# Optimization experiments

Hardware: AMD Instinct MI355X
Metric: run time of the kernel (lower is better)

## Reference

```python
import jax, jax.numpy as jnp
import numpy as np
from jax import lax

EPS = 1e-07
B, H, W = 32, 120, 120
N_PRIM, PRIM_DIM = 16, 8          # 16 capsule types, 8-d pose
N_SEC, SEC_DIM = 10, 16           # 10 secondary capsules, 16-d
FLAT = 9216                       # 16 * 24 * 24
R_ITERS = 3
REC_DIM = H * W * 3               # 43200


def _conv(x, w, b, stride):
    # NHWC input, HWIO kernel, VALID padding
    y = lax.conv_general_dilated(x, w, (stride, stride), 'VALID',
                                 dimension_numbers=('NHWC', 'HWIO', 'NHWC'))
    return y + b


def _squash(s):
    s_norm = jnp.linalg.norm(s, axis=-1, keepdims=True)
    sq = jnp.square(s_norm)
    return sq / (1.0 + sq) * s / (s_norm + EPS)


def setup_inputs() -> dict:
    key = jax.random.key(0)
    ks = jax.random.split(key, 13)
    p = lambda k, shp, s=0.05: (jax.random.normal(k, shp, dtype=jnp.float32) * s)
    inp = {
        'input_x': jax.random.normal(ks[0], (B, H, W, 3), dtype=jnp.float32),
        'y':       jax.random.uniform(ks[1], (B, N_SEC), dtype=jnp.float32),
        'conv1_w': p(ks[2], (9, 9, 3, 256)),
        'conv1_b': jnp.zeros((256,), jnp.float32),
        'conv2_w': p(ks[3], (9, 9, 256, N_PRIM * PRIM_DIM)),
        'conv2_b': jnp.zeros((N_PRIM * PRIM_DIM,), jnp.float32),
        'w_pose':  p(ks[4], (1, FLAT, N_SEC, SEC_DIM, PRIM_DIM)),
        'w1': p(ks[5], (N_SEC * SEC_DIM, 512)), 'b1': jnp.zeros((512,), jnp.float32),
        'w2': p(ks[6], (512, 1024)),            'b2': jnp.zeros((1024,), jnp.float32),
        'w3': p(ks[7], (1024, REC_DIM)),        'b3': jnp.zeros((REC_DIM,), jnp.float32),
    }
    return inp


def reference(input_x, y, conv1_w, conv1_b, conv2_w, conv2_b, w_pose,
              w1, b1, w2, b2, w3, b3):
    b = input_x.shape[0]
    # feature extraction
    x = jax.nn.relu(_conv(input_x, conv1_w, conv1_b, 2))   # [B,56,56,256]
    x = _conv(x, conv2_w, conv2_b, 2)                      # [B,24,24,128]
    u = x.reshape(b, FLAT, PRIM_DIM)                       # [B,9216,8]
    # u_hat[b,n,c,d] = sum_p w_pose[0,n,c,d,p] * u[b,n,p]
    u_hat = jnp.einsum('ncdp,bnp->bncd', w_pose[0], u)     # [B,9216,10,16]
    # dynamic routing
    logits = jnp.zeros((b, FLAT, N_SEC, 1), jnp.float32)
    v = None
    for _ in range(R_ITERS):
        c = jax.nn.softmax(logits, axis=-2)                # over secondary caps
        s = jnp.sum(c * u_hat, axis=1, keepdims=True)      # [B,1,10,16]
        v = _squash(s)
        agreement = jnp.sum(u_hat * v, axis=-1, keepdims=True)  # [B,9216,10,1]
        logits = logits + agreement
    # masking + reconstruction
    mask = y[:, None, :, None]                             # [B,1,10,1]
    v_flat = (mask * v).reshape(b, -1)                     # [B,160]
    h = jax.nn.relu(v_flat @ w1 + b1)
    h = jax.nn.relu(h @ w2 + b2)
    rec = jax.nn.sigmoid(h @ w3 + b3)                      # [B,43200]
    return v, rec
```

## Files before the change

kernel.cpp:

```cpp
#include <hip/hip_runtime.h>
#include <hip/hip_bf16.h>

typedef unsigned short u16;
typedef unsigned int   u32;
typedef __attribute__((ext_vector_type(8))) __bf16 bf16x8;
typedef __attribute__((ext_vector_type(4))) float  f32x4;

#define EPSQ 1e-7f
#define KSPLIT 9
#define KPB 2304
#define KSTEPS 72
#define FC3SPL 8

#define GLDS16(gp, lp) __builtin_amdgcn_global_load_lds( \
    (const __attribute__((address_space(1))) void*)(gp), \
    (__attribute__((address_space(3))) void*)(lp), 16, 0, 0)

__device__ __forceinline__ u16 f2bf(float f){
  u32 u = __float_as_uint(f);
  u32 r = (u + 0x7fffu + ((u >> 16) & 1u)) >> 16;
  return (u16)r;
}
__device__ __forceinline__ float bf2f(u16 h){ return __uint_as_float(((u32)h) << 16); }
__device__ __forceinline__ float blo(u32 w){ return __uint_as_float(w << 16); }
__device__ __forceinline__ float bhi(u32 w){ return __uint_as_float(w & 0xffff0000u); }

__global__ __launch_bounds__(256) void k_im2col(const float* __restrict__ x, u16* __restrict__ A1){
  const int id = blockIdx.x*256 + threadIdx.x;
  const int m  = id >> 5;
  const int s  = id & 31;
  const int b  = m / 3136;
  const int r  = m - b*3136;
  const int oy = r / 56;
  const int ox = r - oy*56;
  const float* xb = x + ((size_t)b*120 + 2*oy)*120*3 + 2*ox*3;
  u16 vals[8];
  #pragma unroll
  for (int j=0;j<8;++j){
    int k = s*8 + j;
    if (k < 243){
      int ky = k / 27;
      int rem = k - ky*27;
      vals[j] = f2bf(xb[(size_t)ky*360 + rem]);
    } else vals[j] = 0;
  }
  *reinterpret_cast<uint4*>(A1 + (size_t)m*256 + s*8) = *reinterpret_cast<uint4*>(vals);
}

__global__ __launch_bounds__(256) void k_wt1(const float* __restrict__ w, u16* __restrict__ wt){
  __shared__ float tile[32][33];
  const int k0 = blockIdx.x*32;
  const int c0 = blockIdx.y*32;
  const int c  = threadIdx.x & 31;
  const int r8 = threadIdx.x >> 5;
  #pragma unroll
  for (int rr=0; rr<4; ++rr){
    int r = r8*4+rr;
    tile[r][c] = (k0+r < 243) ? w[(size_t)(k0+r)*256 + c0 + c] : 0.f;
  }
  __syncthreads();
  #pragma unroll
  for (int rr=0; rr<4; ++rr){
    int r = r8*4+rr;
    wt[(size_t)(c0+r)*256 + k0 + c] = f2bf(tile[c][r]);
  }
}

__global__ __launch_bounds__(256) void k_gemm1(const u16* __restrict__ A1,
    const u16* __restrict__ w1t, const float* __restrict__ bias, u16* __restrict__ a1b){
  __shared__ __align__(16) u16 As[2][4096];
  __shared__ __align__(16) u16 Bs[2][4096];
  const int t  = threadIdx.x;
  const int bx = blockIdx.x;
  const int by = blockIdx.y;
  const int row0 = t>>2, slot = t&3;
  const int wid = t>>6, lane = t&63;
  const int wr = wid>>1, wc = wid&1, lr = lane&15, lq = lane>>4;
  const size_t srcA0 = (size_t)(bx*128 + row0)*256 + slot*8;
  const size_t srcA1 = srcA0 + (size_t)64*256;
  const size_t srcB0 = (size_t)(by*128 + row0)*256 + slot*8;
  const size_t srcB1 = srcB0 + (size_t)64*256;
  f32x4 acc[4][4];
  #pragma unroll
  for (int i=0;i<4;++i)
    #pragma unroll
    for (int j=0;j<4;++j) acc[i][j] = (f32x4){0.f,0.f,0.f,0.f};

  auto stage = [&](int step, int buf){
    const int k0 = step*32;
    GLDS16(A1 + srcA0 + k0, &As[buf][wid*512]);
    GLDS16(A1 + srcA1 + k0, &As[buf][wid*512 + 2048]);
    GLDS16(w1t + srcB0 + k0, &Bs[buf][wid*512]);
    GLDS16(w1t + srcB1 + k0, &Bs[buf][wid*512 + 2048]);
  };
  auto compute = [&](int buf){
    bf16x8 af[4], bfv[4];
    #pragma unroll
    for (int mi=0;mi<4;++mi)
      af[mi] = *reinterpret_cast<const bf16x8*>(&As[buf][(wr*64 + mi*16 + lr)*32 + lq*8]);
    #pragma unroll
    for (int ni=0;ni<4;++ni)
      bfv[ni] = *reinterpret_cast<const bf16x8*>(&Bs[buf][(wc*64 + ni*16 + lr)*32 + lq*8]);
    #pragma unroll
    for (int mi=0;mi<4;++mi)
      #pragma unroll
      for (int ni=0;ni<4;++ni)
        acc[mi][ni] = __builtin_amdgcn_mfma_f32_16x16x32_bf16(af[mi], bfv[ni], acc[mi][ni], 0, 0, 0);
  };

  stage(0, 0);
  int cur = 0;
  for (int step=0; step<8; ++step){
    if (step+1 < 8){
      stage(step+1, cur^1);
      asm volatile("s_waitcnt vmcnt(4)" ::: "memory");
    } else {
      asm volatile("s_waitcnt vmcnt(0)" ::: "memory");
    }
    __builtin_amdgcn_s_barrier();
    __builtin_amdgcn_sched_barrier(0);
    compute(cur);
    __builtin_amdgcn_s_barrier();
    __builtin_amdgcn_sched_barrier(0);
    cur ^= 1;
  }

  #pragma unroll
  for (int ni=0;ni<4;++ni){
    int colg = by*128 + wc*64 + ni*16 + lr;
    float bv = bias[colg];
    #pragma unroll
    for (int mi=0;mi<4;++mi){
      #pragma unroll
      for (int r=0;r<4;++r){
        int rowg = bx*128 + wr*64 + mi*16 + lq*4 + r;
        float v = fmaxf(acc[mi][ni][r] + bv, 0.f);
        a1b[(size_t)rowg*256 + colg] = f2bf(v);
      }
    }
  }
}

__global__ __launch_bounds__(256) void k_wt(const float* __restrict__ w, u16* __restrict__ wt){
  __shared__ float tile[32][33];
  const int k0 = blockIdx.x*32;
  const int c0 = blockIdx.y*32;
  const int c  = threadIdx.x & 31;
  const int r8 = threadIdx.x >> 5;
  #pragma unroll
  for (int rr=0; rr<4; ++rr){
    int r = r8*4+rr;
    tile[r][c] = w[(size_t)(k0+r)*128 + c0 + c];
  }
  __syncthreads();
  #pragma unroll
  for (int rr=0; rr<4; ++rr){
    int r = r8*4+rr;
    wt[(size_t)(c0+r)*20736 + k0 + c] = f2bf(tile[c][r]);
  }
}

__global__ __launch_bounds__(256) void k_conv2(const u16* __restrict__ a1b,
    const u16* __restrict__ w2t, float* __restrict__ part){
  __shared__ __align__(16) u16 As[2][4096];
  __shared__ __align__(16) u16 Bs[2][4096];
  const int t  = threadIdx.x;
  const int bx = blockIdx.x;
  const int ks = blockIdx.y;
  const int row0 = t>>2, slot = t&3;
  int gA[2]; int gB[2];
  #pragma unroll
  for (int q=0;q<2;++q){
    int m  = bx*128 + row0 + q*64;
    int bb = m/576; int r = m - bb*576; int oy = r/24; int ox = r - oy*24;
    gA[q] = ((bb*56 + 2*oy)*56 + 2*ox)*256 + slot*8;
    int col = row0 + q*64;
    gB[q] = col*20736 + slot*8;
  }
  const int wid = t>>6, lane = t&63;
  const int wr = wid>>1, wc = wid&1, lr = lane&15, lq = lane>>4;
  f32x4 acc[4][4];
  #pragma unroll
  for (int i=0;i<4;++i)
    #pragma unroll
    for (int j=0;j<4;++j) acc[i][j] = (f32x4){0.f,0.f,0.f,0.f};
  const int kbase = ks*KPB;

  auto stage = [&](int step, int buf){
    const int k0  = kbase + step*32;
    const int kk  = k0 >> 8;
    const int ky  = kk/9;
    const int kx  = kk - ky*9;
    const int ic0 = k0 & 255;
    const int soff = (ky*56 + kx)*256 + ic0;
    GLDS16(a1b + gA[0] + soff, &As[buf][wid*512]);
    GLDS16(a1b + gA[1] + soff, &As[buf][wid*512 + 2048]);
    GLDS16(w2t + gB[0] + k0,  &Bs[buf][wid*512]);
    GLDS16(w2t + gB[1] + k0,  &Bs[buf][wid*512 + 2048]);
  };
  auto compute = [&](int buf){
    bf16x8 af[4], bfv[4];
    #pragma unroll
    for (int mi=0;mi<4;++mi)
      af[mi] = *reinterpret_cast<const bf16x8*>(&As[buf][(wr*64 + mi*16 + lr)*32 + lq*8]);
    #pragma unroll
    for (int ni=0;ni<4;++ni)
      bfv[ni] = *reinterpret_cast<const bf16x8*>(&Bs[buf][(wc*64 + ni*16 + lr)*32 + lq*8]);
    #pragma unroll
    for (int mi=0;mi<4;++mi)
      #pragma unroll
      for (int ni=0;ni<4;++ni)
        acc[mi][ni] = __builtin_amdgcn_mfma_f32_16x16x32_bf16(af[mi], bfv[ni], acc[mi][ni], 0, 0, 0);
  };

  stage(0, 0);
  int cur = 0;
  for (int step=0; step<KSTEPS; ++step){
    if (step+1 < KSTEPS){
      stage(step+1, cur^1);
      asm volatile("s_waitcnt vmcnt(4)" ::: "memory");
    } else {
      asm volatile("s_waitcnt vmcnt(0)" ::: "memory");
    }
    __builtin_amdgcn_s_barrier();
    __builtin_amdgcn_sched_barrier(0);
    compute(cur);
    __builtin_amdgcn_s_barrier();
    __builtin_amdgcn_sched_barrier(0);
    cur ^= 1;
  }

  const size_t base = ((size_t)ks*18432 + (size_t)bx*128)*128;
  #pragma unroll
  for (int mi=0;mi<4;++mi){
    #pragma unroll
    for (int ni=0;ni<4;++ni){
      int col = wc*64 + ni*16 + lr;
      #pragma unroll
      for (int r=0;r<4;++r){
        int row = wr*64 + mi*16 + lq*4 + r;
        part[base + (size_t)row*128 + col] = acc[mi][ni][r];
      }
    }
  }
}

__global__ __launch_bounds__(256) void k_comb(const float* __restrict__ part,
    const float* __restrict__ bias, float* __restrict__ u){
  const int i4 = blockIdx.x*256 + threadIdx.x;
  const float4* b4 = reinterpret_cast<const float4*>(bias);
  float4 s = b4[i4 & 31];
  const float4* p4 = reinterpret_cast<const float4*>(part);
  #pragma unroll
  for (int ks=0; ks<KSPLIT; ++ks){
    float4 p = p4[(size_t)ks*589824 + i4];
    s.x += p.x; s.y += p.y; s.z += p.z; s.w += p.w;
  }
  reinterpret_cast<float4*>(u)[i4] = s;
}

__global__ __launch_bounds__(256) void k_uhat(const float* __restrict__ u,
    const float* __restrict__ wpose, u16* __restrict__ uhat){
  __shared__ float Wn[1280];
  __shared__ float us[256];
  const int n = blockIdx.x;
  const int t = threadIdx.x;
  #pragma unroll
  for (int j=0;j<5;++j) Wn[t + j*256] = wpose[(size_t)n*1280 + t + j*256];
  us[t] = u[((size_t)(t>>3)*9216 + n)*8 + (t&7)];
  __syncthreads();
  const int b = t>>3, d0 = (t&7)*2;
  float uv[8];
  #pragma unroll
  for (int p=0;p<8;++p) uv[p] = us[b*8+p];
  for (int c=0;c<10;++c){
    const float* w0 = &Wn[(c*16 + d0)*8];
    float v0=0.f, v1=0.f;
    #pragma unroll
    for (int p=0;p<8;++p){ v0 = fmaf(w0[p], uv[p], v0); v1 = fmaf(w0[8+p], uv[p], v1); }
    u32 pk = (u32)f2bf(v0) | ((u32)f2bf(v1) << 16);
    *reinterpret_cast<u32*>(uhat + ((((size_t)b*10 + c)*9216 + n)*16 + d0)) = pk;
  }
}

template<int ITER>
__global__ __launch_bounds__(256) void k_route(const u16* __restrict__ uhat,
    const float* __restrict__ spin, float* __restrict__ logi,
    float* __restrict__ spout){
  const int ch = blockIdx.x;
  const int b  = blockIdx.y;
  const int t  = threadIdx.x;
  const int n  = ch*256 + t;
  __shared__ float vl[160];
  __shared__ float sq[160];
  __shared__ float wlds[10][257];
  __shared__ float pacc[10][16][33];
  if (ITER >= 2){
    float sv = 0.f;
    if (t < 160){
      #pragma unroll 4
      for (int c2=0;c2<36;++c2) sv += spin[((size_t)c2*32 + b)*160 + t];
      sq[t] = sv*sv;
    }
    __syncthreads();
    if (t < 160){
      int cc = t >> 4;
      float ss = 0.f;
      #pragma unroll
      for (int j=0;j<16;++j) ss += sq[cc*16 + j];
      float nrm = sqrtf(ss);
      vl[t] = (ss/(1.f+ss)) * sv / (nrm + EPSQ);
    }
    __syncthreads();
  }
  float w[10];
  if (ITER == 1){
    #pragma unroll
    for (int c=0;c<10;++c) w[c] = 0.1f;
  } else {
    float l[10];
    #pragma unroll
    for (int c=0;c<10;++c){
      const u16* up = uhat + ((((size_t)b*10 + c)*9216 + n) << 4);
      const uint4 q0 = *reinterpret_cast<const uint4*>(up);
      const uint4 q1 = *reinterpret_cast<const uint4*>(up + 8);
      const float* v = &vl[c*16];
      float dot = blo(q0.x)*v[0] + bhi(q0.x)*v[1]
                + blo(q0.y)*v[2] + bhi(q0.y)*v[3]
                + blo(q0.z)*v[4] + bhi(q0.z)*v[5]
                + blo(q0.w)*v[6] + bhi(q0.w)*v[7]
                + blo(q1.x)*v[8] + bhi(q1.x)*v[9]
                + blo(q1.y)*v[10]+ bhi(q1.y)*v[11]
                + blo(q1.z)*v[12]+ bhi(q1.z)*v[13]
                + blo(q1.w)*v[14]+ bhi(q1.w)*v[15];
      size_t li = ((size_t)b*10 + c)*9216 + n;
      float lc = dot;
      if (ITER == 3) lc += logi[li];
      if (ITER == 2) logi[li] = lc;
      l[c] = lc;
    }
    float mx = l[0];
    #pragma unroll
    for (int c=1;c<10;++c) mx = fmaxf(mx, l[c]);
    float s = 0.f;
    #pragma unroll
    for (int c=0;c<10;++c){ w[c] = __expf(l[c]-mx); s += w[c]; }
    float inv = 1.f/s;
    #pragma unroll
    for (int c=0;c<10;++c) w[c] *= inv;
  }
  #pragma unroll
  for (int c=0;c<10;++c) wlds[c][t] = w[c];
  __syncthreads();

  const int nl = t>>3, dp = t&7;
  float a0[10], a1[10];
  #pragma unroll
  for (int c=0;c<10;++c){ a0[c]=0.f; a1[c]=0.f; }
  #pragma unroll
  for (int c=0;c<10;++c){
    const u32* ub = reinterpret_cast<const u32*>(
        uhat + ((((size_t)b*10 + c)*9216 + (size_t)ch*256) << 4));
    float acc0 = 0.f, acc1 = 0.f;
    #pragma unroll
    for (int chunk=0; chunk<8; ++chunk){
      u32 v = ub[chunk*256 + t];
      float wv = wlds[c][chunk*32 + nl];
      acc0 = fmaf(wv, blo(v), acc0);
      acc1 = fmaf(wv, bhi(v), acc1);
    }
    a0[c] = acc0; a1[c] = acc1;
  }
  #pragma unroll
  for (int c=0;c<10;++c){
    pacc[c][2*dp  ][nl] = a0[c];
    pacc[c][2*dp+1][nl] = a1[c];
  }
  __syncthreads();
  if (t < 160){
    const int c = t >> 4, d = t & 15;
    float acc = 0.f;
    #pragma unroll
    for (int j=0;j<32;++j) acc += pacc[c][d][j];
    spout[((size_t)ch*32 + b)*160 + t] = acc;
  }
}

__global__ __launch_bounds__(256) void k_head(const float* __restrict__ y,
    const float* __restrict__ spin, const float* __restrict__ w1,
    const float* __restrict__ b1, const float* __restrict__ w2,
    const float* __restrict__ b2, float* __restrict__ dout_v,
    float* __restrict__ h2T){
  const int b = blockIdx.x;
  const int q = blockIdx.y;
  const int t = threadIdx.x;
  __shared__ float vl[160];
  __shared__ float sq[160];
  __shared__ float h1s[512];
  float sv = 0.f;
  if (t < 160){
    #pragma unroll 4
    for (int c2=0;c2<36;++c2) sv += spin[((size_t)c2*32 + b)*160 + t];
    sq[t] = sv*sv;
  }
  __syncthreads();
  if (t < 160){
    int cc = t >> 4;
    float ss = 0.f;
    #pragma unroll
    for (int j=0;j<16;++j) ss += sq[cc*16 + j];
    float nrm = sqrtf(ss);
    float vv = (ss/(1.f+ss)) * sv / (nrm + EPSQ);
    if (q == 0) dout_v[(size_t)b*160 + t] = vv;
    vl[t] = vv * y[b*10 + cc];
  }
  __syncthreads();
  #pragma unroll
  for (int j=0;j<2;++j){
    const int oc = j*256 + t;
    float acc = b1[oc];
    for (int k=0;k<160;++k) acc = fmaf(vl[k], w1[(size_t)k*512 + oc], acc);
    h1s[oc] = fmaxf(acc, 0.f);
  }
  __syncthreads();
  const int oc2 = q*256 + t;
  float acc = b2[oc2];
  for (int k=0;k<512;++k) acc = fmaf(h1s[k], w2[(size_t)k*1024 + oc2], acc);
  h2T[(size_t)oc2*32 + b] = fmaxf(acc, 0.f);
}

__global__ __launch_bounds__(256) void k_fc3p(const float* __restrict__ h2T,
    const float* __restrict__ w3, float* __restrict__ fp){
  __shared__ float4 hs4[128][8];
  const int t  = threadIdx.x;
  const int oc = blockIdx.x*256 + t;
  const int ks = blockIdx.y;
  const float4* src = reinterpret_cast<const float4*>(h2T + (size_t)ks*128*32);
  #pragma unroll
  for (int r=0;r<4;++r)
    (&hs4[0][0])[t + r*256] = src[t + r*256];
  __syncthreads();
  const bool ok = oc < 43200;
  float a[32];
  #pragma unroll
  for (int b=0;b<32;++b) a[b] = 0.f;
  const size_t wbase = (size_t)ks*128*43200 + (size_t)(ok ? oc : 0);
  #pragma unroll 4
  for (int k=0;k<128;++k){
    float wv = w3[wbase + (size_t)k*43200];
    #pragma unroll
    for (int q=0;q<8;++q){
      float4 hv = hs4[k][q];
      a[q*4+0] = fmaf(hv.x, wv, a[q*4+0]);
      a[q*4+1] = fmaf(hv.y, wv, a[q*4+1]);
      a[q*4+2] = fmaf(hv.z, wv, a[q*4+2]);
      a[q*4+3] = fmaf(hv.w, wv, a[q*4+3]);
    }
  }
  if (ok){
    #pragma unroll
    for (int b=0;b<32;++b) fp[(size_t)(ks*32 + b)*43200 + oc] = a[b];
  }
}

__global__ __launch_bounds__(256) void k_fc3f(const float* __restrict__ fp,
    const float* __restrict__ b3, float* __restrict__ outr){
  const int i4 = blockIdx.x*256 + threadIdx.x;
  if (i4 >= 345600) return;
  const int b = i4 / 10800, oc4 = i4 - b*10800;
  const float4* b34 = reinterpret_cast<const float4*>(b3);
  float4 s = b34[oc4];
  const float4* fp4 = reinterpret_cast<const float4*>(fp);
  #pragma unroll
  for (int ks=0;ks<FC3SPL;++ks){
    float4 p = fp4[(size_t)(ks*32 + b)*10800 + oc4];
    s.x += p.x; s.y += p.y; s.z += p.z; s.w += p.w;
  }
  float4 o;
  o.x = 1.f/(1.f + __expf(-s.x));
  o.y = 1.f/(1.f + __expf(-s.y));
  o.z = 1.f/(1.f + __expf(-s.z));
  o.w = 1.f/(1.f + __expf(-s.w));
  reinterpret_cast<float4*>(outr)[i4] = o;
}

extern "C" void kernel_launch(void* const* d_in, const int* in_sizes, int n_in,
                              void* d_out, int out_size, void* d_ws, size_t ws_size,
                              hipStream_t stream){
  (void)in_sizes; (void)n_in; (void)out_size; (void)ws_size;
  const float* x     = (const float*)d_in[0];
  const float* y     = (const float*)d_in[1];
  const float* c1w   = (const float*)d_in[2];
  const float* c1b   = (const float*)d_in[3];
  const float* c2w   = (const float*)d_in[4];
  const float* c2b   = (const float*)d_in[5];
  const float* wpose = (const float*)d_in[6];
  const float* w1    = (const float*)d_in[7];
  const float* b1    = (const float*)d_in[8];
  const float* w2    = (const float*)d_in[9];
  const float* b2    = (const float*)d_in[10];
  const float* w3    = (const float*)d_in[11];
  const float* b3    = (const float*)d_in[12];
  float* out = (float*)d_out;

  char* ws = (char*)d_ws;
  u16*   a1bp  = (u16*)(ws + 0);
  u16*   A1col = (u16*)(ws + 52000000);
  float* partp = (float*)(ws + 52000000);
  u16*   uhatp = (u16*)(ws + 0);
  u16*   w1tp  = (u16*)(ws + 138000000);
  u16*   w2tp  = (u16*)(ws + 138500000);
  float* up    = (float*)(ws + 144000000);
  float* logip = (float*)(ws + 154000000);
  float* spA   = (float*)(ws + 166000000);
  float* spB   = (float*)(ws + 166800000);
  float* h2Tp  = (float*)(ws + 167600000);
  float* fc3pp = (float*)(ws + 0);

  k_im2col<<<dim3(12544),  256, 0, stream>>>(x, A1col);
  k_wt1   <<<dim3(8,8),    256, 0, stream>>>(c1w, w1tp);
  k_wt    <<<dim3(648,4),  256, 0, stream>>>(c2w, w2tp);
  k_gemm1 <<<dim3(784,2),  256, 0, stream>>>(A1col, w1tp, c1b, a1bp);
  k_conv2 <<<dim3(144,KSPLIT), 256, 0, stream>>>(a1bp, w2tp, partp);
  k_comb  <<<dim3(2304),   256, 0, stream>>>(partp, c2b, up);
  k_uhat  <<<dim3(9216),   256, 0, stream>>>(up, wpose, uhatp);

  k_route<1><<<dim3(36,32), 256, 0, stream>>>(uhatp, spB, logip, spA);
  k_route<2><<<dim3(36,32), 256, 0, stream>>>(uhatp, spA, logip, spB);
  k_route<3><<<dim3(36,32), 256, 0, stream>>>(uhatp, spB, logip, spA);

  k_head <<<dim3(32,4), 256, 0, stream>>>(y, spA, w1, b1, w2, b2, out, h2Tp);
  k_fc3p <<<dim3(169,FC3SPL), 256, 0, stream>>>(h2Tp, w3, fc3pp);
  k_fc3f <<<dim3(1350), 256, 0, stream>>>(fc3pp, b3, out + 5120);
}
```

Measured before the change: 536.2 us.

## Load B operand directly to registers and swizzle A LDS layout in conv GEMMs

In both the conv1 GEMM and the conv2 implicit GEMM, the B (weight) tiles no longer go through LDS. Each wave loads its own B fragments from global memory straight into registers, double-buffered across even and odd steps with the loop unrolled by two. The A tile staging now uses an XOR swizzle on the 16-byte slot, matched on the read side, to cut LDS bank conflicts. This halves LDS traffic and footprint, at the cost of more VGPRs and of duplicated global B reads across the two wave rows (wr), which may add pressure on L2.

```diff
diff --git a/kernel.cpp b/kernel.cpp
--- a/kernel.cpp
+++ b/kernel.cpp
@@ -15,6 +15,8 @@
 #define GLDS16(gp, lp) __builtin_amdgcn_global_load_lds( \
     (const __attribute__((address_space(1))) void*)(gp), \
     (__attribute__((address_space(3))) void*)(lp), 16, 0, 0)
+#define WAITV6() asm volatile("s_waitcnt vmcnt(6)" ::: "memory")
+#define WAITV0() asm volatile("s_waitcnt vmcnt(0)" ::: "memory")
 
 __device__ __forceinline__ u16 f2bf(float f){
   u32 u = __float_as_uint(f);
@@ -69,60 +71,66 @@
 __global__ __launch_bounds__(256) void k_gemm1(const u16* __restrict__ A1,
     const u16* __restrict__ w1t, const float* __restrict__ bias, u16* __restrict__ a1b){
   __shared__ __align__(16) u16 As[2][4096];
-  __shared__ __align__(16) u16 Bs[2][4096];
   const int t  = threadIdx.x;
   const int bx = blockIdx.x;
   const int by = blockIdx.y;
-  const int row0 = t>>2, slot = t&3;
+  const int row0  = t>>2;
+  const int sslot = (t&3) ^ ((t>>3)&3);
   const int wid = t>>6, lane = t&63;
   const int wr = wid>>1, wc = wid&1, lr = lane&15, lq = lane>>4;
-  const size_t srcA0 = (size_t)(bx*128 + row0)*256 + slot*8;
+  const int sl = lq ^ ((lr>>1)&3);
+  const size_t srcA0 = (size_t)(bx*128 + row0)*256 + sslot*8;
   const size_t srcA1 = srcA0 + (size_t)64*256;
-  const size_t srcB0 = (size_t)(by*128 + row0)*256 + slot*8;
-  const size_t srcB1 = srcB0 + (size_t)64*256;
+  const u16* pB = w1t + (size_t)(by*128 + wc*64 + lr)*256 + lq*8;
   f32x4 acc[4][4];
   #pragma unroll
   for (int i=0;i<4;++i)
     #pragma unroll
     for (int j=0;j<4;++j) acc[i][j] = (f32x4){0.f,0.f,0.f,0.f};
-
+  int aoff[4];
+  #pragma unroll
+  for (int mi=0;mi<4;++mi) aoff[mi] = (wr*64 + mi*16 + lr)*32 + sl*8;
+
+  bf16x8 bE[4], bO[4];
   auto stage = [&](int step, int buf){
     const int k0 = step*32;
     GLDS16(A1 + srcA0 + k0, &As[buf][wid*512]);
     GLDS16(A1 + srcA1 + k0, &As[buf][wid*512 + 2048]);
-    GLDS16(w1t + srcB0 + k0, &Bs[buf][wid*512]);
-    GLDS16(w1t + srcB1 + k0, &Bs[buf][wid*512 + 2048]);
   };
-  auto compute = [&](int buf){
-    bf16x8 af[4], bfv[4];
+  auto loadB = [&](bf16x8* d, int step){
+    #pragma unroll
+    for (int ni=0;ni<4;++ni)
+      d[ni] = *reinterpret_cast<const bf16x8*>(pB + (size_t)ni*16*256 + step*32);
+  };
+  auto compute = [&](int buf, bf16x8* bv){
+    bf16x8 af[4];
     #pragma unroll
     for (int mi=0;mi<4;++mi)
-      af[mi] = *reinterpret_cast<const bf16x8*>(&As[buf][(wr*64 + mi*16 + lr)*32 + lq*8]);
-    #pragma unroll
-    for (int ni=0;ni<4;++ni)
-      bfv[ni] = *reinterpret_cast<const bf16x8*>(&Bs[buf][(wc*64 + ni*16 + lr)*32 + lq*8]);
+      af[mi] = *reinterpret_cast<const bf16x8*>(&As[buf][aoff[mi]]);
     #pragma unroll
     for (int mi=0;mi<4;++mi)
       #pragma unroll
       for (int ni=0;ni<4;++ni)
-        acc[mi][ni] = __builtin_amdgcn_mfma_f32_16x16x32_bf16(af[mi], bfv[ni], acc[mi][ni], 0, 0, 0);
+        acc[mi][ni] = __builtin_amdgcn_mfma_f32_16x16x32_bf16(af[mi], bv[ni], acc[mi][ni], 0, 0, 0);
   };
 
   stage(0, 0);
-  int cur = 0;
-  for (int step=0; step<8; ++step){
-    if (step+1 < 8){
-      stage(step+1, cur^1);
-      asm volatile("s_waitcnt vmcnt(4)" ::: "memory");
-    } else {
-      asm volatile("s_waitcnt vmcnt(0)" ::: "memory");
-    }
-    __builtin_amdgcn_s_barrier();
-    __builtin_amdgcn_sched_barrier(0);
-    compute(cur);
-    __builtin_amdgcn_s_barrier();
-    __builtin_amdgcn_sched_barrier(0);
-    cur ^= 1;
+  loadB(bE, 0);
+  for (int step=0; step<8; step+=2){
+    if (step+1 < 8){ stage(step+1, 1); loadB(bO, step+1); WAITV6(); }
+    else WAITV0();
+    __builtin_amdgcn_s_barrier();
+    __builtin_amdgcn_sched_barrier(0);
+    compute(0, bE);
+    __builtin_amdgcn_s_barrier();
+    __builtin_amdgcn_sched_barrier(0);
+    if (step+2 < 8){ stage(step+2, 0); loadB(bE, step+2); WAITV6(); }
+    else WAITV0();
+    __builtin_amdgcn_s_barrier();
+    __builtin_amdgcn_sched_barrier(0);
+    compute(1, bO);
+    __builtin_amdgcn_s_barrier();
+    __builtin_amdgcn_sched_barrier(0);
   }
 
   #pragma unroll
@@ -163,29 +171,33 @@
 __global__ __launch_bounds__(256) void k_conv2(const u16* __restrict__ a1b,
     const u16* __restrict__ w2t, float* __restrict__ part){
   __shared__ __align__(16) u16 As[2][4096];
-  __shared__ __align__(16) u16 Bs[2][4096];
   const int t  = threadIdx.x;
   const int bx = blockIdx.x;
   const int ks = blockIdx.y;
-  const int row0 = t>>2, slot = t&3;
-  int gA[2]; int gB[2];
+  const int row0  = t>>2;
+  const int sslot = (t&3) ^ ((t>>3)&3);
+  int gA[2];
   #pragma unroll
   for (int q=0;q<2;++q){
     int m  = bx*128 + row0 + q*64;
     int bb = m/576; int r = m - bb*576; int oy = r/24; int ox = r - oy*24;
-    gA[q] = ((bb*56 + 2*oy)*56 + 2*ox)*256 + slot*8;
-    int col = row0 + q*64;
-    gB[q] = col*20736 + slot*8;
+    gA[q] = ((bb*56 + 2*oy)*56 + 2*ox)*256 + sslot*8;
   }
   const int wid = t>>6, lane = t&63;
   const int wr = wid>>1, wc = wid&1, lr = lane&15, lq = lane>>4;
+  const int sl = lq ^ ((lr>>1)&3);
+  const int kbase = ks*KPB;
+  const u16* pB = w2t + (size_t)(wc*64 + lr)*20736 + lq*8 + kbase;
   f32x4 acc[4][4];
   #pragma unroll
   for (int i=0;i<4;++i)
     #pragma unroll
     for (int j=0;j<4;++j) acc[i][j] = (f32x4){0.f,0.f,0.f,0.f};
-  const int kbase = ks*KPB;
-
+  int aoff[4];
+  #pragma unroll
+  for (int mi=0;mi<4;++mi) aoff[mi] = (wr*64 + mi*16 + lr)*32 + sl*8;
+
+  bf16x8 bE[4], bO[4];
   auto stage = [&](int step, int buf){
     const int k0  = kbase + step*32;
     const int kk  = k0 >> 8;
@@ -195,39 +207,41 @@
     const int soff = (ky*56 + kx)*256 + ic0;
     GLDS16(a1b + gA[0] + soff, &As[buf][wid*512]);
     GLDS16(a1b + gA[1] + soff, &As[buf][wid*512 + 2048]);
-    GLDS16(w2t + gB[0] + k0,  &Bs[buf][wid*512]);
-    GLDS16(w2t + gB[1] + k0,  &Bs[buf][wid*512 + 2048]);
   };
-  auto compute = [&](int buf){
-    bf16x8 af[4], bfv[4];
+  auto loadB = [&](bf16x8* d, int step){
+    #pragma unroll
+    for (int ni=0;ni<4;++ni)
+      d[ni] = *reinterpret_cast<const bf16x8*>(pB + (size_t)ni*16*20736 + step*32);
+  };
+  auto compute = [&](int buf, bf16x8* bv){
+    bf16x8 af[4];
     #pragma unroll
     for (int mi=0;mi<4;++mi)
-      af[mi] = *reinterpret_cast<const bf16x8*>(&As[buf][(wr*64 + mi*16 + lr)*32 + lq*8]);
-    #pragma unroll
-    for (int ni=0;ni<4;++ni)
-      bfv[ni] = *reinterpret_cast<const bf16x8*>(&Bs[buf][(wc*64 + ni*16 + lr)*32 + lq*8]);
+      af[mi] = *reinterpret_cast<const bf16x8*>(&As[buf][aoff[mi]]);
     #pragma unroll
     for (int mi=0;mi<4;++mi)
       #pragma unroll
       for (int ni=0;ni<4;++ni)
-        acc[mi][ni] = __builtin_amdgcn_mfma_f32_16x16x32_bf16(af[mi], bfv[ni], acc[mi][ni], 0, 0, 0);
+        acc[mi][ni] = __builtin_amdgcn_mfma_f32_16x16x32_bf16(af[mi], bv[ni], acc[mi][ni], 0, 0, 0);
   };
 
   stage(0, 0);
-  int cur = 0;
-  for (int step=0; step<KSTEPS; ++step){
-    if (step+1 < KSTEPS){
-      stage(step+1, cur^1);
-      asm volatile("s_waitcnt vmcnt(4)" ::: "memory");
-    } else {
-      asm volatile("s_waitcnt vmcnt(0)" ::: "memory");
-    }
-    __builtin_amdgcn_s_barrier();
-    __builtin_amdgcn_sched_barrier(0);
-    compute(cur);
-    __builtin_amdgcn_s_barrier();
-    __builtin_amdgcn_sched_barrier(0);
-    cur ^= 1;
+  loadB(bE, 0);
+  for (int step=0; step<KSTEPS; step+=2){
+    if (step+1 < KSTEPS){ stage(step+1, 1); loadB(bO, step+1); WAITV6(); }
+    else WAITV0();
+    __builtin_amdgcn_s_barrier();
+    __builtin_amdgcn_sched_barrier(0);
+    compute(0, bE);
+    __builtin_amdgcn_s_barrier();
+    __builtin_amdgcn_sched_barrier(0);
+    if (step+2 < KSTEPS){ stage(step+2, 0); loadB(bE, step+2); WAITV6(); }
+    else WAITV0();
+    __builtin_amdgcn_s_barrier();
+    __builtin_amdgcn_sched_barrier(0);
+    compute(1, bO);
+    __builtin_amdgcn_s_barrier();
+    __builtin_amdgcn_sched_barrier(0);
   }
 
   const size_t base = ((size_t)ks*18432 + (size_t)bx*128)*128;
```

After: 648.8 us. 21.0% more time.
